# Optimization experiments

Hardware: AMD Instinct MI355X
Metric: run time of the kernel (lower is better)

## Reference

```python
import jax, jax.numpy as jnp
import numpy as np

N_QUBITS = 14
LATENT = 14
DEPTH = 4
BATCH = 256
DIM = 1 << N_QUBITS  # 16384 amplitudes

# PennyLane convention: wire 0 is the most-significant bit of the flat state index.
_idx = np.arange(DIM)
_bits = (_idx[None, :] >> (N_QUBITS - 1 - np.arange(N_QUBITS)[:, None])) & 1  # [n_qubits, DIM]
_parity = np.sum(_bits[:-1] * _bits[1:], axis=0) % 2  # adjacent-pair CZ chain parity
CZ_SIGNS = jnp.asarray(1.0 - 2.0 * _parity, dtype=jnp.complex64)  # [DIM]
Z_SIGNS = jnp.asarray(1 - 2 * _bits[:LATENT], dtype=jnp.float32)  # [LATENT, DIM]


def _rx(t):
    c = jnp.cos(0.5 * t) + 0j
    s = -1j * jnp.sin(0.5 * t)
    m = jnp.stack([jnp.stack([c, s], -1), jnp.stack([s, c], -1)], -2)
    return m.astype(jnp.complex64)


def _ry(t):
    c = jnp.cos(0.5 * t)
    s = jnp.sin(0.5 * t)
    m = jnp.stack([jnp.stack([c, -s], -1), jnp.stack([s, c], -1)], -2)
    return m.astype(jnp.complex64)


def _rz(t):
    e = jnp.exp(-0.5j * t.astype(jnp.complex64))
    z = jnp.zeros_like(e)
    m = jnp.stack([jnp.stack([e, z], -1), jnp.stack([z, jnp.conj(e)], -1)], -2)
    return m.astype(jnp.complex64)


def _apply_1q(state, mat, wire):
    # state: [B, DIM]; mat: [2,2] (shared) or [B,2,2] (per-sample)
    B = state.shape[0]
    left = 1 << wire
    right = 1 << (N_QUBITS - wire - 1)
    st = state.reshape(B, left, 2, right)
    if mat.ndim == 3:
        st = jnp.einsum('bij,bajc->baic', mat, st)
    else:
        st = jnp.einsum('ij,bajc->baic', mat, st)
    return st.reshape(B, DIM)


def setup_inputs() -> dict:
    key = jax.random.key(0)
    k1, k2, k3, k4 = jax.random.split(key, 4)
    conditioning = jax.random.normal(k1, (BATCH, LATENT), dtype=jnp.float32)
    lim = 1.0 / np.sqrt(LATENT)
    W_enc = jax.random.uniform(k2, (N_QUBITS, LATENT), jnp.float32, -lim, lim)
    b_enc = jax.random.uniform(k3, (N_QUBITS,), jnp.float32, -lim, lim)
    # TorchLayer default init: U(0, 2*pi)
    weights = jax.random.uniform(k4, (DEPTH, N_QUBITS, 3), jnp.float32, 0.0, 2.0 * np.pi)
    return {"conditioning": conditioning, "W_enc": W_enc, "b_enc": b_enc, "weights": weights}


def reference(conditioning, W_enc, b_enc, weights):
    # encode: Linear + SiLU -> per-wire rotation angles [B, n_qubits]
    emb = conditioning @ W_enc.T + b_enc
    emb = emb * jax.nn.sigmoid(emb)
    B = emb.shape[0]

    state = jnp.zeros((B, DIM), jnp.complex64).at[:, 0].set(1.0)

    # angle encoding: RX(v) then RY(v) on each wire (per-sample gates)
    for w in range(N_QUBITS):
        v = emb[:, w]
        U = jnp.einsum('bij,bjk->bik', _ry(v), _rx(v))  # [B,2,2]
        state = _apply_1q(state, U, w)

    # variational layers: RZ, RX, RY per wire (shared gates), then CZ chain
    for d in range(DEPTH):
        for w in range(N_QUBITS):
            p = weights[d, w]
            U = _ry(p[2]) @ _rx(p[1]) @ _rz(p[0])  # [2,2]
            state = _apply_1q(state, U, w)
        state = state * CZ_SIGNS  # all adjacent CZs fused into one diagonal

    probs = state.real ** 2 + state.imag ** 2  # [B, DIM]
    latent = probs @ Z_SIGNS.T  # <Z_w> for w in range(LATENT) -> [B, LATENT]

    # F.layer_norm over last dim, no affine params
    mu = jnp.mean(latent, axis=-1, keepdims=True)
    var = jnp.var(latent, axis=-1, keepdims=True)
    return (latent - mu) / jnp.sqrt(var + 1e-5)
```

## Files before the change

kernel.cpp:

```cpp
#include <hip/hip_runtime.h>
#include <math.h>

#define NQ    14
#define DIM   16384
#define DEPTH 4

typedef __attribute__((ext_vector_type(2))) float f2;
typedef __attribute__((ext_vector_type(4))) float f4;

__device__ __forceinline__ f2 cmul(f2 a, f2 b) {
    return (f2){a.x*b.x - a.y*b.y, a.x*b.y + a.y*b.x};
}
__device__ __forceinline__ f2 cmac2(f2 x, f2 u, f2 us, f2 y, f2 v, f2 vs) {
    f2 r = x.xx * u;
    r += x.yy * us;
    r += y.xx * v;
    r += y.yy * vs;
    return r;
}


template<int CTRL>
__device__ __forceinline__ f2 dpp2(f2 v) {
    union U { f2 f; int i[2]; } u, r;
    u.f = v;
    r.i[0] = __builtin_amdgcn_update_dpp(0, u.i[0], CTRL, 0xF, 0xF, true);
    r.i[1] = __builtin_amdgcn_update_dpp(0, u.i[1], CTRL, 0xF, 0xF, true);
    return r.f;
}
template<int XB> __device__ __forceinline__ f2 lxchg(f2 v);
template<> __device__ __forceinline__ f2 lxchg<1>(f2 v) { return dpp2<0xB1>(v); }
template<> __device__ __forceinline__ f2 lxchg<2>(f2 v) { return dpp2<0x4E>(v); }
template<> __device__ __forceinline__ f2 lxchg<8>(f2 v) { return dpp2<0x128>(v); }

template<int MASK>
__device__ __forceinline__ void reg_gate(f2 a[16], const f4* G) {
    f4 g0 = G[0], g1 = G[1], g2 = G[2], g3 = G[3];
    #pragma unroll
    for (int l = 0; l < 16; ++l) {
        if (l & MASK) continue;
        const int j = l | MASK;
        f2 x = a[l], y = a[j];
        a[l] = cmac2(x, g0.xy, g0.zw, y, g1.xy, g1.zw);
        a[j] = cmac2(x, g2.xy, g2.zw, y, g3.xy, g3.zw);
    }
}

template<int XB>
__device__ __forceinline__ void lane_gate(f2 a[16], const f4* G, int t) {
    const bool hi = (t & XB) != 0;
    f4 c1 = G[hi ? 3 : 0];
    f4 c2 = G[hi ? 2 : 1];
    #pragma unroll
    for (int l = 0; l < 16; ++l) {
        f2 p = lxchg<XB>(a[l]);
        a[l] = cmac2(a[l], c1.xy, c1.zw, p, c2.xy, c2.zw);
    }
}

__device__ __forceinline__ void cz_A(f2 a[16], int t) {
    const int n = t & 63, w = t >> 6;
    const int pT = (__popc(w & (w >> 1)) + __popc(n & (n >> 1)) + ((n & 1) & (w >> 3))) & 1;
    const float F0 = pT ? -1.f : 1.f;
    const float F1 = (pT ^ ((n >> 5) & 1)) ? -1.f : 1.f;
    #pragma unroll
    for (int l = 0; l < 16; ++l) {
        float s = (l & 1) ? F1 : F0;
        if (__popc(l & (l >> 1)) & 1) s = -s;
        a[l] *= s;
    }
}

__device__ __forceinline__ void cz_B(f2 a[16], int t) {
    const int n = t & 63, w = t >> 6;
    const int n0 = n & 1, n1 = (n >> 1) & 1, n2 = (n >> 2) & 1;
    const int n3 = (n >> 3) & 1, n4 = (n >> 4) & 1, n5 = (n >> 5) & 1;
    const int pT = ((n2 & n4) ^ (n4 & n0) ^ (n0 & n5) ^ (n5 & n1) ^ (n1 & n3)
                    ^ (n3 & (w & 1)) ^ (__popc(w & (w >> 1)) & 1));
    const float F0 = pT ? -1.f : 1.f;
    const float F1 = (pT ^ n2) ? -1.f : 1.f;
    #pragma unroll
    for (int l = 0; l < 16; ++l) {
        float s = (l & 8) ? F1 : F0;
        if (__popc(l & (l >> 1)) & 1) s = -s;
        a[l] *= s;
    }
}

__global__ __launch_bounds__(1024)
void qlg_kernel(const float* __restrict__ cond,
                const float* __restrict__ Wenc,
                const float* __restrict__ benc,
                const float* __restrict__ wts,
                float* __restrict__ out)
{
    __shared__ f2 st[DIM];
    __shared__ f4 gtab[6][7][4];
    __shared__ f4 gates0[NQ][2];
    __shared__ f2 qv[NQ][2];
    __shared__ f2 Phi[128];
    __shared__ f2 Plo[128];
    __shared__ float embS[NQ];
    __shared__ float wred[16][NQ];
    __shared__ float lat[NQ];

    const int b = blockIdx.x;
    const int t = threadIdx.x;
    const int n = t & 63, w = t >> 6;
    const int bB = (w << 10)
                 | (((n >> 3) & 1) << 5) | (((n >> 1) & 1) << 4)
                 | (((n >> 5) & 1) << 3) | ((n & 1) << 2)
                 | (((n >> 4) & 1) << 1) | ((n >> 2) & 1);

    if (t < NQ) {
        float s = benc[t];
        #pragma unroll
        for (int k = 0; k < NQ; ++k) s += cond[b*NQ + k] * Wenc[t*NQ + k];
        embS[t] = s / (1.0f + __expf(-s));
    }
    if (t >= 64 && t < 64 + DEPTH*NQ) {
        const int gi = t - 64;
        const int d = gi / NQ, ww = gi % NQ;
        const float p0 = wts[(d*NQ + ww)*3 + 0];
        const float p1 = wts[(d*NQ + ww)*3 + 1];
        const float p2 = wts[(d*NQ + ww)*3 + 2];
        float s0, c0, s1, c1, s2, c2;
        sincosf(0.5f*p0, &s0, &c0);
        sincosf(0.5f*p1, &s1, &c1);
        sincosf(0.5f*p2, &s2, &c2);
        f2 e0  = (f2){c0, -s0};
        f2 e0c = (f2){c0,  s0};
        f2 is1 = (f2){0.f, -s1};
        f2 m00 = c1 * e0;
        f2 m01 = cmul(is1, e0c);
        f2 m10 = cmul(is1, e0);
        f2 m11 = c1 * e0c;
        f2 u00 = c2*m00 - s2*m10;
        f2 u01 = c2*m01 - s2*m11;
        f2 u10 = s2*m00 + c2*m10;
        f2 u11 = s2*m01 + c2*m11;
        if (d == 0) {
            gates0[ww][0] = (f4){u00.x, u00.y, u01.x, u01.y};
            gates0[ww][1] = (f4){u10.x, u10.y, u11.x, u11.y};
        } else {
            const bool isA = (ww <= 3) || (ww == 6) || (ww == 8) || (ww == 9);
            int slot;
            if (isA) slot = (ww <= 3) ? ww : (ww == 6 ? 4 : (ww == 8 ? 5 : 6));
            else     slot = (ww >= 10) ? (ww - 10) : (ww == 4 ? 4 : (ww == 5 ? 5 : 6));
            const int h = (d == 1) ? (isA ? 0 : 1)
                        : (d == 2) ? (isA ? 3 : 2)
                                   : (isA ? 4 : 5);
            gtab[h][slot][0] = (f4){u00.x, u00.y, -u00.y, u00.x};
            gtab[h][slot][1] = (f4){u01.x, u01.y, -u01.y, u01.x};
            gtab[h][slot][2] = (f4){u10.x, u10.y, -u10.y, u10.x};
            gtab[h][slot][3] = (f4){u11.x, u11.y, -u11.y, u11.x};
        }
    }
    __syncthreads();

    if (t < NQ) {
        float v = embS[t];
        float s, c;
        sincosf(0.5f*v, &s, &c);
        f2 a0 = (f2){c*c,  s*s};
        f2 a1 = (f2){s*c, -s*c};
        f4 va = gates0[t][0], vb = gates0[t][1];
        f2 u00 = (f2){va.x, va.y}, u01 = (f2){va.z, va.w};
        f2 u10 = (f2){vb.x, vb.y}, u11 = (f2){vb.z, vb.w};
        qv[t][0] = cmul(u00, a0) + cmul(u01, a1);
        qv[t][1] = cmul(u10, a0) + cmul(u11, a1);
    }
    __syncthreads();

    if (t < 128) {
        f2 p = qv[0][(t >> 6) & 1];
        #pragma unroll
        for (int ww = 1; ww <= 6; ++ww) p = cmul(p, qv[ww][(t >> (6 - ww)) & 1]);
        Phi[t] = p;
    } else if (t < 256) {
        const int j = t - 128;
        f2 p = qv[7][(j >> 6) & 1];
        #pragma unroll
        for (int ww = 8; ww <= 13; ++ww) p = cmul(p, qv[ww][(j >> (13 - ww)) & 1]);
        Plo[j] = p;
    }
    __syncthreads();

    f2 a[16];
    {
        f2 plo = Plo[((n & 7) << 4) | w];
        #pragma unroll
        for (int l = 0; l < 16; ++l)
            a[l] = cmul(Phi[(l << 3) | (n >> 3)], plo);
        cz_A(a, t);
    }

    #pragma unroll 1
    for (int h = 0; h < 6; ++h) {
        const f4 (*g)[4] = gtab[h];
        reg_gate<8>(a, g[0]);
        reg_gate<4>(a, g[1]);
        reg_gate<2>(a, g[2]);
        reg_gate<1>(a, g[3]);
        lane_gate<8>(a, g[4], t);
        lane_gate<2>(a, g[5], t);
        lane_gate<1>(a, g[6], t);
        if (h == 1)      cz_B(a, t);
        else if (h == 3) cz_A(a, t);
        if (h == 0 || h == 4) {
            #pragma unroll
            for (int l = 0; l < 16; ++l) st[t + (l << 10)] = a[l];
            __syncthreads();
            #pragma unroll
            for (int l = 0; l < 16; ++l) a[l] = st[bB + (l << 6)];
        } else if (h == 2) {
            #pragma unroll
            for (int l = 0; l < 16; ++l) st[bB + (l << 6)] = a[l];
            __syncthreads();
            #pragma unroll
            for (int l = 0; l < 16; ++l) a[l] = st[t + (l << 10)];
        }
    }

    float SU, Q10, Q11, Q12, Q13;
    {
        SU = Q10 = Q11 = Q12 = Q13 = 0.f;
        #pragma unroll
        for (int l = 0; l < 16; ++l) {
            float p = a[l].x*a[l].x + a[l].y*a[l].y;
            SU  += p;
            Q10 += (l & 8) ? -p : p;
            Q11 += (l & 4) ? -p : p;
            Q12 += (l & 2) ? -p : p;
            Q13 += (l & 1) ? -p : p;
        }
    }

    {
        const int lane = t & 63, wv = t >> 6;
        const int sbit[10] = {9, 8, 7, 6, 3, 1, 5, 0, 4, 2};
        #pragma unroll
        for (int ww = 0; ww < NQ; ++ww) {
            float v;
            if      (ww == 10) v = Q10;
            else if (ww == 11) v = Q11;
            else if (ww == 12) v = Q12;
            else if (ww == 13) v = Q13;
            else               v = ((t >> sbit[ww]) & 1) ? -SU : SU;
            #pragma unroll
            for (int off = 32; off > 0; off >>= 1) v += __shfl_down(v, off, 64);
            if (lane == 0) wred[wv][ww] = v;
        }
    }
    __syncthreads();
    if (t < NQ) {
        float s = 0.f;
        #pragma unroll
        for (int k = 0; k < 16; ++k) s += wred[k][t];
        lat[t] = s;
    }
    __syncthreads();
    if (t < NQ) {
        float mu = 0.f;
        #pragma unroll
        for (int k = 0; k < NQ; ++k) mu += lat[k];
        mu *= (1.0f / NQ);
        float var = 0.f;
        #pragma unroll
        for (int k = 0; k < NQ; ++k) { float dv = lat[k] - mu; var += dv*dv; }
        var *= (1.0f / NQ);
        out[b*NQ + t] = (lat[t] - mu) * rsqrtf(var + 1e-5f);
    }
}

extern "C" void kernel_launch(void* const* d_in, const int* in_sizes, int n_in,
                              void* d_out, int out_size, void* d_ws, size_t ws_size,
                              hipStream_t stream)
{
    (void)n_in; (void)d_ws; (void)ws_size; (void)out_size;
    const float* cond = (const float*)d_in[0];
    const float* Wenc = (const float*)d_in[1];
    const float* benc = (const float*)d_in[2];
    const float* wts  = (const float*)d_in[3];
    float* out = (float*)d_out;
    const int B = in_sizes[0] / NQ;
    qlg_kernel<<<dim3(B), dim3(1024), 0, stream>>>(cond, Wenc, benc, wts, out);
}
```

Measured before the change: 99.00 us.

## Precompute shared gate matrices in a prep kernel and read them from global memory

Moves the per-layer variational gate construction (sincos and matrix products) out of every block into a single small prep kernel that writes the gate table to workspace. The main kernel now reads gate coefficients from global memory through restrict pointers, which can become scalar or cached loads, and the h loop is fully unrolled so the gate addresses are compile-time constants. This removes redundant trig work and LDS gate reads in each of the 256 blocks. In exchange it adds a second kernel launch and a dependence on the workspace buffer, and the full unroll may raise register pressure or code size.

New measurement: 93.70 us. 5.3% less time.

```diff
diff --git a/kernel.cpp b/kernel.cpp
--- a/kernel.cpp
+++ b/kernel.cpp
@@ -34,7 +34,7 @@
 template<> __device__ __forceinline__ f2 lxchg<8>(f2 v) { return dpp2<0x128>(v); }
 
 template<int MASK>
-__device__ __forceinline__ void reg_gate(f2 a[16], const f4* G) {
+__device__ __forceinline__ void reg_gate(f2 a[16], const f4* __restrict__ G) {
     f4 g0 = G[0], g1 = G[1], g2 = G[2], g3 = G[3];
     #pragma unroll
     for (int l = 0; l < 16; ++l) {
@@ -47,7 +47,7 @@
 }
 
 template<int XB>
-__device__ __forceinline__ void lane_gate(f2 a[16], const f4* G, int t) {
+__device__ __forceinline__ void lane_gate(f2 a[16], const f4* __restrict__ G, int t) {
     const bool hi = (t & XB) != 0;
     f4 c1 = G[hi ? 3 : 0];
     f4 c2 = G[hi ? 2 : 1];
@@ -87,16 +87,57 @@
     }
 }
 
+__global__ void qlg_prep(const float* __restrict__ wts,
+                         f4* __restrict__ G)
+{
+    const int t = threadIdx.x;
+    if (t >= DEPTH * NQ) return;
+    const int d = t / NQ, ww = t % NQ;
+    const float p0 = wts[(d*NQ + ww)*3 + 0];
+    const float p1 = wts[(d*NQ + ww)*3 + 1];
+    const float p2 = wts[(d*NQ + ww)*3 + 2];
+    float s0, c0, s1, c1, s2, c2;
+    sincosf(0.5f*p0, &s0, &c0);
+    sincosf(0.5f*p1, &s1, &c1);
+    sincosf(0.5f*p2, &s2, &c2);
+    f2 e0  = (f2){c0, -s0};
+    f2 e0c = (f2){c0,  s0};
+    f2 is1 = (f2){0.f, -s1};
+    f2 m00 = c1 * e0;
+    f2 m01 = cmul(is1, e0c);
+    f2 m10 = cmul(is1, e0);
+    f2 m11 = c1 * e0c;
+    f2 u00 = c2*m00 - s2*m10;
+    f2 u01 = c2*m01 - s2*m11;
+    f2 u10 = s2*m00 + c2*m10;
+    f2 u11 = s2*m01 + c2*m11;
+    if (d == 0) {
+        G[168 + ww*2 + 0] = (f4){u00.x, u00.y, u01.x, u01.y};
+        G[168 + ww*2 + 1] = (f4){u10.x, u10.y, u11.x, u11.y};
+    } else {
+        const bool isA = (ww <= 3) || (ww == 6) || (ww == 8) || (ww == 9);
+        int slot;
+        if (isA) slot = (ww <= 3) ? ww : (ww == 6 ? 4 : (ww == 8 ? 5 : 6));
+        else     slot = (ww >= 10) ? (ww - 10) : (ww == 4 ? 4 : (ww == 5 ? 5 : 6));
+        const int h = (d == 1) ? (isA ? 0 : 1)
+                    : (d == 2) ? (isA ? 3 : 2)
+                               : (isA ? 4 : 5);
+        const int base = (h*7 + slot)*4;
+        G[base + 0] = (f4){u00.x, u00.y, -u00.y, u00.x};
+        G[base + 1] = (f4){u01.x, u01.y, -u01.y, u01.x};
+        G[base + 2] = (f4){u10.x, u10.y, -u10.y, u10.x};
+        G[base + 3] = (f4){u11.x, u11.y, -u11.y, u11.x};
+    }
+}
+
 __global__ __launch_bounds__(1024)
 void qlg_kernel(const float* __restrict__ cond,
                 const float* __restrict__ Wenc,
                 const float* __restrict__ benc,
-                const float* __restrict__ wts,
+                const f4* __restrict__ gG,
                 float* __restrict__ out)
 {
     __shared__ f2 st[DIM];
-    __shared__ f4 gtab[6][7][4];
-    __shared__ f4 gates0[NQ][2];
     __shared__ f2 qv[NQ][2];
     __shared__ f2 Phi[128];
     __shared__ f2 Plo[128];
@@ -116,45 +157,8 @@
         float s = benc[t];
         #pragma unroll
         for (int k = 0; k < NQ; ++k) s += cond[b*NQ + k] * Wenc[t*NQ + k];
-        embS[t] = s / (1.0f + __expf(-s));
-    }
-    if (t >= 64 && t < 64 + DEPTH*NQ) {
-        const int gi = t - 64;
-        const int d = gi / NQ, ww = gi % NQ;
-        const float p0 = wts[(d*NQ + ww)*3 + 0];
-        const float p1 = wts[(d*NQ + ww)*3 + 1];
-        const float p2 = wts[(d*NQ + ww)*3 + 2];
-        float s0, c0, s1, c1, s2, c2;
-        sincosf(0.5f*p0, &s0, &c0);
-        sincosf(0.5f*p1, &s1, &c1);
-        sincosf(0.5f*p2, &s2, &c2);
-        f2 e0  = (f2){c0, -s0};
-        f2 e0c = (f2){c0,  s0};
-        f2 is1 = (f2){0.f, -s1};
-        f2 m00 = c1 * e0;
-        f2 m01 = cmul(is1, e0c);
-        f2 m10 = cmul(is1, e0);
-        f2 m11 = c1 * e0c;
-        f2 u00 = c2*m00 - s2*m10;
-        f2 u01 = c2*m01 - s2*m11;
-        f2 u10 = s2*m00 + c2*m10;
-        f2 u11 = s2*m01 + c2*m11;
-        if (d == 0) {
-            gates0[ww][0] = (f4){u00.x, u00.y, u01.x, u01.y};
-            gates0[ww][1] = (f4){u10.x, u10.y, u11.x, u11.y};
-        } else {
-            const bool isA = (ww <= 3) || (ww == 6) || (ww == 8) || (ww == 9);
-            int slot;
-            if (isA) slot = (ww <= 3) ? ww : (ww == 6 ? 4 : (ww == 8 ? 5 : 6));
-            else     slot = (ww >= 10) ? (ww - 10) : (ww == 4 ? 4 : (ww == 5 ? 5 : 6));
-            const int h = (d == 1) ? (isA ? 0 : 1)
-                        : (d == 2) ? (isA ? 3 : 2)
-                                   : (isA ? 4 : 5);
-            gtab[h][slot][0] = (f4){u00.x, u00.y, -u00.y, u00.x};
-            gtab[h][slot][1] = (f4){u01.x, u01.y, -u01.y, u01.x};
-            gtab[h][slot][2] = (f4){u10.x, u10.y, -u10.y, u10.x};
-            gtab[h][slot][3] = (f4){u11.x, u11.y, -u11.y, u11.x};
-        }
+        float e = s / (1.0f + __expf(-s));
+        embS[t] = e;
     }
     __syncthreads();
 
@@ -164,7 +168,7 @@
         sincosf(0.5f*v, &s, &c);
         f2 a0 = (f2){c*c,  s*s};
         f2 a1 = (f2){s*c, -s*c};
-        f4 va = gates0[t][0], vb = gates0[t][1];
+        f4 va = gG[168 + t*2], vb = gG[168 + t*2 + 1];
         f2 u00 = (f2){va.x, va.y}, u01 = (f2){va.z, va.w};
         f2 u10 = (f2){vb.x, vb.y}, u11 = (f2){vb.z, vb.w};
         qv[t][0] = cmul(u00, a0) + cmul(u01, a1);
@@ -195,16 +199,16 @@
         cz_A(a, t);
     }
 
-    #pragma unroll 1
+    #pragma unroll
     for (int h = 0; h < 6; ++h) {
-        const f4 (*g)[4] = gtab[h];
-        reg_gate<8>(a, g[0]);
-        reg_gate<4>(a, g[1]);
-        reg_gate<2>(a, g[2]);
-        reg_gate<1>(a, g[3]);
-        lane_gate<8>(a, g[4], t);
-        lane_gate<2>(a, g[5], t);
-        lane_gate<1>(a, g[6], t);
+        const f4* __restrict__ g = gG + h*7*4;
+        reg_gate<8>(a, g + 0*4);
+        reg_gate<4>(a, g + 1*4);
+        reg_gate<2>(a, g + 2*4);
+        reg_gate<1>(a, g + 3*4);
+        lane_gate<8>(a, g + 4*4, t);
+        lane_gate<2>(a, g + 5*4, t);
+        lane_gate<1>(a, g + 6*4, t);
         if (h == 1)      cz_B(a, t);
         else if (h == 3) cz_A(a, t);
         if (h == 0 || h == 4) {
@@ -277,12 +281,14 @@
                               void* d_out, int out_size, void* d_ws, size_t ws_size,
                               hipStream_t stream)
 {
-    (void)n_in; (void)d_ws; (void)ws_size; (void)out_size;
+    (void)n_in; (void)ws_size; (void)out_size;
     const float* cond = (const float*)d_in[0];
     const float* Wenc = (const float*)d_in[1];
     const float* benc = (const float*)d_in[2];
     const float* wts  = (const float*)d_in[3];
     float* out = (float*)d_out;
+    f4* G = (f4*)d_ws;
     const int B = in_sizes[0] / NQ;
-    qlg_kernel<<<dim3(B), dim3(1024), 0, stream>>>(cond, Wenc, benc, wts, out);
-}
+    qlg_prep<<<dim3(1), dim3(64), 0, stream>>>(wts, G);
+    qlg_kernel<<<dim3(B), dim3(1024), 0, stream>>>(cond, Wenc, benc, G, out);
+}
```
